# Performance work log

Hardware: AMD Instinct MI355X
Metric: run time of the kernel (lower is better)

Reference implementation:

```python
import jax, jax.numpy as jnp
import numpy as np

NEG = -1e30  # log-space 'zero' (avoid actual -inf for stable grads)
BLANK = 1


def _ctc_single(logp, target, il, tl):
    # logp: [T, V] log-probabilities; target: [S] int; il, tl: scalar lengths
    T, V = logp.shape
    S = target.shape[0]
    L = 2 * S + 1
    # extended label sequence: blank, t0, blank, t1, ..., blank
    ext = jnp.full((L,), BLANK, dtype=target.dtype).at[1::2].set(target)
    prev2 = jnp.concatenate([jnp.full((2,), -1, dtype=ext.dtype), ext[:-2]])
    can_skip = (ext != BLANK) & (ext != prev2)  # allowed s-2 transition
    valid = jnp.arange(L) < (2 * tl + 1)  # mask lattice positions beyond target length
    lp_ext = logp[:, ext]  # [T, L] gather of emission log-probs along the lattice

    alpha0 = jnp.full((L,), NEG, dtype=logp.dtype)
    alpha0 = alpha0.at[0].set(lp_ext[0, 0]).at[1].set(lp_ext[0, 1])
    alpha0 = jnp.where(valid, alpha0, NEG)

    def step(alpha, inp):
        t, lp = inp  # lp: [L]
        a1 = jnp.concatenate([jnp.full((1,), NEG, alpha.dtype), alpha[:-1]])
        a2 = jnp.concatenate([jnp.full((2,), NEG, alpha.dtype), alpha[:-2]])
        a2 = jnp.where(can_skip, a2, NEG)
        new = jnp.logaddexp(jnp.logaddexp(alpha, a1), a2) + lp
        new = jnp.where(valid, new, NEG)
        new = jnp.where(t < il, new, alpha)  # freeze alpha past input length
        return new, None

    alpha, _ = jax.lax.scan(step, alpha0, (jnp.arange(1, T), lp_ext[1:]))
    end = 2 * tl
    ll = jnp.logaddexp(alpha[end], alpha[end - 1])
    loss = -ll
    # zero_infinity=True: clamp non-finite / degenerate losses to 0
    loss = jnp.where(loss < 1e29, loss, 0.0)
    return loss


def setup_inputs() -> dict:
    key = jax.random.key(0)
    k1, k2, k3, k4 = jax.random.split(key, 4)
    B, T, V, S = 64, 2000, 256, 400
    # module expects log-probabilities over phonemes
    log_probs = jax.nn.log_softmax(
        jax.random.normal(k1, (B, T, V), dtype=jnp.float32), axis=-1)
    # targets avoid blank_id=1 (labels in [2, V))
    targets = jax.random.randint(k2, (B, S), 2, V, dtype=jnp.int32)
    input_lengths = jax.random.randint(k3, (B,), T // 2, T + 1, dtype=jnp.int32)
    target_lengths = jax.random.randint(k4, (B,), S // 2, S + 1, dtype=jnp.int32)
    return {"log_probs": log_probs, "targets": targets,
            "input_lengths": input_lengths, "target_lengths": target_lengths}


def reference(log_probs, targets, input_lengths, target_lengths):
    losses = jax.vmap(_ctc_single)(log_probs, targets, input_lengths, target_lengths)
    # nn.CTCLoss reduction='mean': per-sample loss divided by target length, then batch mean
    return jnp.mean(losses / target_lengths.astype(losses.dtype))
```

## Files before the change

kernel.cpp:

```cpp
#include <hip/hip_runtime.h>

#define LOG2E 1.4426950408889634f
#define LN2   0.6931471805599453f

namespace {
constexpr int B    = 64;
constexpr int T    = 2000;
constexpr int V    = 256;
constexpr int S    = 400;
constexpr int CHK  = 8;
constexpr int NCTP = 250;
constexpr int KP   = 408;
constexpr size_t GELEM  = (size_t)B * NCTP * KP * 8;
constexpr size_t GBYTES = GELEM * 2;
constexpr size_t LAOFF  = GBYTES / 4;
constexpr size_t LGOFF  = LAOFF + 64 * 1024;
constexpr size_t REQBYTES = GBYTES + 2 * 64 * 1024 * 4;
constexpr int LSTR = 260;
constexpr int NW7  = 7;
constexpr int NCT7 = 250;
constexpr int BST7 = 12;
}

using h8 = __attribute__((ext_vector_type(8))) _Float16;

__device__ __forceinline__ float fexp2(float x){ return __builtin_amdgcn_exp2f(x); }
__device__ __forceinline__ float flog2(float x){ return __builtin_amdgcn_logf(x); }

__device__ __forceinline__ float wave_shr1(float x) {
  int v = __builtin_amdgcn_update_dpp(0, __builtin_bit_cast(int, x),
                                      0x138, 0xf, 0xf, true);
  return __builtin_bit_cast(float, v);
}
__device__ __forceinline__ int wave_shr1_i(int x) {
  return __builtin_amdgcn_update_dpp(0, x, 0x138, 0xf, 0xf, true);
}
__device__ __forceinline__ float wave_shl1(float x) {
  int v = __builtin_amdgcn_update_dpp(0, __builtin_bit_cast(int, x),
                                      0x130, 0xf, 0xf, true);
  return __builtin_bit_cast(float, v);
}
__device__ __forceinline__ int wave_shl1_i(int x) {
  return __builtin_amdgcn_update_dpp(0, x, 0x130, 0xf, 0xf, true);
}

__global__ __launch_bounds__(512)
void ctc_gather_kernel(const float* __restrict__ logp,
                       const int* __restrict__ targets,
                       _Float16* __restrict__ G)
{
  const int tile = blockIdx.x;
  const int b    = blockIdx.y;
  const int tid  = threadIdx.x;
  const int i0   = tile * 64;
  const float* lp = logp + (size_t)b * T * V;
  const int*   tg = targets + (size_t)b * S;

  __shared__ float ls[64 * LSTR];
  __shared__ int   tgs[S];

  for (int f = tid; f < 64 * 64; f += 512) {
    const int row = f >> 6, c4 = f & 63;
    int t = i0 + 1 + row; if (t > T - 1) t = T - 1;
    float4 v = ((const float4*)(lp + (size_t)t * V))[c4];
    *(float4*)&ls[row * LSTR + c4 * 4] = v;
  }
  for (int k = tid; k < S; k += 512) tgs[k] = tg[k];
  __syncthreads();

  const int w    = tid >> 6;
  const int lane = tid & 63;
  _Float16* gb = G + (size_t)b * NCTP * KP * 8;

  for (int it = w; it < 56; it += 8) {
    const int kb = it >> 3;
    const int cc = it & 7;
    const int c  = tile * 8 + cc;
    if (c >= NCTP) continue;
    const int k = kb * 64 + lane;
    if (k >= KP) continue;
    const int e = (k < S) ? tgs[k] : 1;
    h8 hv;
    #pragma unroll
    for (int j = 0; j < 8; ++j)
      hv[j] = (_Float16)fexp2(ls[(cc * 8 + j) * LSTR + e] * LOG2E);
    *(h8*)(gb + ((size_t)c * KP + k) * 8) = hv;
  }
}

__global__ __launch_bounds__(64)
void ctc_fb_kernel(const float* __restrict__ logp,
                   const int* __restrict__ targets,
                   const int* __restrict__ input_len,
                   const int* __restrict__ target_len,
                   const _Float16* __restrict__ G,
                   float* __restrict__ la,
                   float* __restrict__ lg)
{
  const int b    = blockIdx.x;
  const int dir  = blockIdx.y;
  const int lane = threadIdx.x & 63;
  const float* __restrict__ lp = logp + (size_t)b * T * V;
  const int il = input_len[b];
  const int tl = target_len[b];
  const int m  = il >> 1;
  const int* tg = targets + (size_t)b * S;

  const _Float16* Gb = G + (size_t)b * NCTP * KP * 8;
  const int krow = (8 * lane < KP - 8) ? 8 * lane : KP - 8;

  float skF[8], skB[8];
  #pragma unroll
  for (int j = 0; j < 8; ++j) {
    const int k   = 8 * lane + j;
    const int kc  = k < S ? k : S - 1;
    const int km  = (k - 1) < 0 ? 0 : ((k - 1) < S ? (k - 1) : S - 1);
    skF[j] = (k > 0 && tg[kc] != tg[km]) ? 1.0f : 0.0f;
    const int k2  = k + 1;
    const int k2c = k2 < S ? k2 : S - 1;
    const int k2m = (k2 - 1) < S ? (k2 - 1) : S - 1;
    skB[j] = (tg[k2c] != tg[k2m]) ? 1.0f : 0.0f;
  }

  h8 bufA[9], bufB[9], bufC[9], bufD[9];

  auto loadch = [&](h8 (&buf)[9], int c2) {
    if (c2 < 0) c2 = 0;
    if (c2 > NCTP - 1) c2 = NCTP - 1;
    const size_t base = (size_t)c2 * (KP * 8);
    #pragma unroll
    for (int j = 0; j < 8; ++j)
      buf[j] = *(const h8*)(Gb + base + (size_t)(krow + j) * 8);
    buf[8] = *(const h8*)(Gb + base + (size_t)400 * 8);
  };

  if (dir == 0) {
    float a[16];
    #pragma unroll
    for (int i = 0; i < 16; ++i) a[i] = 0.0f;
    int  E = 0;
    bool alive = (lane == 0);
    if (lane == 0) {
      a[0] = fexp2(lp[1] * LOG2E);
      a[1] = fexp2(lp[tg[0]] * LOG2E);
    }

    auto fwd_sub = [&](h8 (&buf)[9], const int c_) {
      float ps[8][8], pb[8];
      #pragma unroll
      for (int j = 0; j < 8; ++j) {
        #pragma unroll
        for (int i = 0; i < 8; ++i) ps[j][i] = (float)buf[j][i];
      }
      #pragma unroll
      for (int i = 0; i < 8; ++i) pb[i] = (float)buf[8][i];
      loadch(buf, c_ + 4);

      const int E1 = wave_shr1_i(E);
      if (!alive) E = E1;
      int d = E1 - E; d = d > 126 ? 126 : (d < -126 ? -126 : d);
      const float f = ldexpf(1.0f, d);

      #pragma unroll
      for (int i = 0; i < 8; ++i) {
        const int t = 1 + c_ * CHK + i;
        if (t <= m) {
          const float h = wave_shr1(a[15]) * f;
          #pragma unroll
          for (int j = 7; j >= 0; --j) {
            const float lo = j ? a[2 * j - 1] : h;
            a[2 * j + 1] = __builtin_fmaf(lo, skF[j],
                                          a[2 * j + 1] + a[2 * j]) * ps[j][i];
            a[2 * j]     = (a[2 * j] + lo) * pb[i];
          }
        }
      }
      {
        float mx[8];
        #pragma unroll
        for (int q = 0; q < 8; ++q) mx[q] = fmaxf(a[2 * q], a[2 * q + 1]);
        #pragma unroll
        for (int q = 0; q < 4; ++q) mx[q] = fmaxf(mx[q], mx[q + 4]);
        const float m2 = fmaxf(fmaxf(mx[0], mx[1]), fmaxf(mx[2], mx[3]));
        int k = 0; (void)frexpf(m2, &k);
        #pragma unroll
        for (int i = 0; i < 16; ++i) a[i] = ldexpf(a[i], -k);
        E += k;
        alive = (m2 != 0.0f);
      }
    };

    loadch(bufA, 0); loadch(bufB, 1); loadch(bufC, 2); loadch(bufD, 3);
    const int NCH = (m + 7) >> 3;
    for (int c = 0; c < NCH; c += 4) {
      fwd_sub(bufA, c);
      fwd_sub(bufB, c + 1);
      fwd_sub(bufC, c + 2);
      fwd_sub(bufD, c + 3);
    }

    float* dst = la + (size_t)b * 1024 + 16 * lane;
    #pragma unroll
    for (int i = 0; i < 16; ++i) dst[i] = flog2(a[i]) + (float)E;
  } else {
    float g[16];
    const int s0 = 16 * lane;
    bool alive = false;
    #pragma unroll
    for (int i = 0; i < 16; ++i) {
      const int s = s0 + i;
      g[i] = (s == 2 * tl || s == 2 * tl - 1) ? 1.0f : 0.0f;
      alive = alive || (g[i] != 0.0f);
    }
    int E = 0;

    const int c_hi = (il - 2) >> 3;
    const int c_lo = m >> 3;

    auto bwd_sub = [&](h8 (&buf)[9], const int c_) {
      float ps[8][8], pb[8];
      #pragma unroll
      for (int j = 0; j < 8; ++j) {
        #pragma unroll
        for (int i = 0; i < 8; ++i) ps[j][i] = (float)buf[j][i];
      }
      #pragma unroll
      for (int i = 0; i < 8; ++i) pb[i] = (float)buf[8][i];
      loadch(buf, c_ - 4);

      const int E1 = wave_shl1_i(E);
      if (!alive) E = E1;
      int d = E1 - E; d = d > 126 ? 126 : (d < -126 ? -126 : d);
      const float f = ldexpf(1.0f, d);

      #pragma unroll
      for (int ii = 0; ii < 8; ++ii) {
        const int i = 7 - ii;
        const int row = 1 + c_ * CHK + i;
        if (row > m && row < il) {
          float pg[16];
          #pragma unroll
          for (int q = 0; q < 8; ++q) {
            pg[2 * q]     = g[2 * q]     * pb[i];
            pg[2 * q + 1] = g[2 * q + 1] * ps[q][i];
          }
          const float h0 = wave_shl1(pg[0]) * f;
          const float h1 = wave_shl1(pg[1]) * f;
          #pragma unroll
          for (int q = 0; q < 8; ++q) {
            const float u1 = (q < 7) ? pg[2 * q + 2] : h0;
            const float u2 = (q < 7) ? pg[2 * q + 3] : h1;
            g[2 * q + 1] = __builtin_fmaf(u2, skB[q], pg[2 * q + 1] + u1);
            g[2 * q]     = pg[2 * q] + pg[2 * q + 1];
          }
        }
      }
      {
        float mx[8];
        #pragma unroll
        for (int q = 0; q < 8; ++q) mx[q] = fmaxf(g[2 * q], g[2 * q + 1]);
        #pragma unroll
        for (int q = 0; q < 4; ++q) mx[q] = fmaxf(mx[q], mx[q + 4]);
        const float m2 = fmaxf(fmaxf(mx[0], mx[1]), fmaxf(mx[2], mx[3]));
        int k = 0; (void)frexpf(m2, &k);
        #pragma unroll
        for (int i = 0; i < 16; ++i) g[i] = ldexpf(g[i], -k);
        E += k;
        alive = (m2 != 0.0f);
      }
    };

    loadch(bufA, c_hi);     loadch(bufB, c_hi - 1);
    loadch(bufC, c_hi - 2); loadch(bufD, c_hi - 3);
    for (int c = c_hi; c >= c_lo; c -= 4) {
      bwd_sub(bufA, c);
      bwd_sub(bufB, c - 1);
      bwd_sub(bufC, c - 2);
      bwd_sub(bufD, c - 3);
    }

    float* dst = lg + (size_t)b * 1024 + 16 * lane;
    #pragma unroll
    for (int i = 0; i < 16; ++i) dst[i] = flog2(g[i]) + (float)E;
  }
}

__global__ __launch_bounds__(64)
void ctc_merge_kernel(const float* __restrict__ la,
                      const float* __restrict__ lg,
                      const int* __restrict__ target_len,
                      float* __restrict__ out)
{
  const int b    = blockIdx.x;
  const int lane = threadIdx.x;
  const int tl = target_len[b];
  const int Lb = 2 * tl + 1;
  const float* A  = la + (size_t)b * 1024;
  const float* Gm = lg + (size_t)b * 1024;

  float vs[16];
  float vmax = -1e30f;
  #pragma unroll
  for (int r = 0; r < 16; ++r) {
    const int s = lane + 64 * r;
    float x = A[s] + Gm[s];
    x = (s < Lb) ? x : -1e30f;
    vs[r] = x;
    vmax = fmaxf(vmax, x);
  }
  #pragma unroll
  for (int o = 32; o > 0; o >>= 1) vmax = fmaxf(vmax, __shfl_xor(vmax, o, 64));
  float sum = 0.0f;
  #pragma unroll
  for (int r = 0; r < 16; ++r) sum += fexp2(vs[r] - vmax);
  #pragma unroll
  for (int o = 32; o > 0; o >>= 1) sum += __shfl_xor(sum, o, 64);
  if (lane == 0) {
    const float ll = (vmax + flog2(sum)) * LN2;
    float loss = -ll;
    if (!(loss < 1e29f)) loss = 0.0f;
    atomicAdd(out, loss / ((float)tl * (float)B));
  }
}

__global__ __launch_bounds__(NW7 * 64)
void ctc_alpha7_kernel(const float* __restrict__ logp,
                       const int* __restrict__ targets,
                       const int* __restrict__ input_len,
                       const int* __restrict__ target_len,
                       float* __restrict__ out)
{
  const int b    = blockIdx.x;
  const int tid  = threadIdx.x;
  const int w    = tid >> 6;
  const int lane = tid & 63;
  const bool lane0 = (lane == 0);
  const float* __restrict__ lp = logp + (size_t)b * T * V;
  const int il = input_len[b];
  const int tl = target_len[b];
  const int Lb = 2 * tl + 1;

  __shared__ float bnd[NW7 - 1][NCT7 * BST7];
  __shared__ int   cnt[NW7 - 1];
  __shared__ float pblk[T];
  __shared__ float afin[NW7 * 64 * 2];

  if (tid < NW7 - 1) cnt[tid] = 0;

  const int* tg = targets + (size_t)b * S;
  const int k1 = (tid < S) ? tid : (S - 1);
  const int e1 = tg[k1];
  const float sk1 = (k1 == 0 || e1 != tg[k1 - 1]) ? 1.0f : 0.0f;

  for (int i = tid; i < T; i += NW7 * 64) {
    int t = (i + 1 < T) ? (i + 1) : (T - 1);
    pblk[i] = fexp2(lp[(size_t)t * V + 1] * LOG2E);
  }
  __syncthreads();

  const bool active = (w * 128) < Lb;
  if (active) {
    float a0 = 0.0f, a1 = 0.0f;
    int   E  = 0;
    if (tid == 0) { a0 = fexp2(lp[1] * LOG2E); a1 = fexp2(lp[e1] * LOG2E); }

    float tokL[CHK];
    #pragma unroll
    for (int i = 0; i < CHK; ++i) tokL[i] = lp[(size_t)(1 + i) * V + e1];

    const int NCH = (il - 1 + CHK - 1) / CHK;
    for (int c = 0; c < NCH; ++c) {
      const int t0 = 1 + c * CHK;
      float tokP[CHK];
      #pragma unroll
      for (int i = 0; i < CHK; ++i) tokP[i] = fexp2(tokL[i] * LOG2E);
      float nl[CHK];
      if (c + 1 < NCT7) {
        #pragma unroll
        for (int i = 0; i < CHK; ++i) {
          int tt = t0 + CHK + i; if (tt > T - 1) tt = T - 1;
          nl[i] = lp[(size_t)tt * V + e1];
        }
      }
      float pbk[CHK];
      {
        float4 q0 = *(const float4*)&pblk[c * CHK];
        float4 q1 = *(const float4*)&pblk[c * CHK + 4];
        pbk[0]=q0.x; pbk[1]=q0.y; pbk[2]=q0.z; pbk[3]=q0.w;
        pbk[4]=q1.x; pbk[5]=q1.y; pbk[6]=q1.z; pbk[7]=q1.w;
      }
      float bq[CHK];
      int Ep = 0;
      if (w > 0) {
        while (__hip_atomic_load(&cnt[w - 1], __ATOMIC_ACQUIRE,
                                 __HIP_MEMORY_SCOPE_WORKGROUP) < c + 1)
          __builtin_amdgcn_s_sleep(1);
        const float* src = &bnd[w - 1][c * BST7];
        float4 q0 = *(const float4*)(src);
        float4 q1 = *(const float4*)(src + 4);
        bq[0]=q0.x; bq[1]=q0.y; bq[2]=q0.z; bq[3]=q0.w;
        bq[4]=q1.x; bq[5]=q1.y; bq[6]=q1.z; bq[7]=q1.w;
        Ep = __float_as_int(src[8]);
      } else {
        #pragma unroll
        for (int i = 0; i < CHK; ++i) bq[i] = 0.0f;
      }
      const float mz  = fmaxf(a0, a1);
      const int   E1o = __shfl_up(E, 1);
      const int   E8  = __shfl_up(E, 8);
      const int   E9  = __shfl_up(E, 9);
      const float mz1 = __shfl_up(mz, 1);
      if (mz == 0.0f) E = (lane < 8) ? Ep : E8;
      int E1 = (mz1 == 0.0f) ? ((lane <= 8) ? Ep : E9) : E1o;
      if (lane0) E1 = (w == 0) ? E : Ep;
      int d = E1 - E; d = d > 126 ? 126 : (d < -126 ? -126 : d);
      const float f = ldexpf(1.0f, d);
      const float a1s = a1;
      float pub[CHK];
      #pragma unroll
      for (int i = 0; i < CHK; ++i) {
        const int t = t0 + i;
        if (t < il) {
          float hl = wave_shr1(a1);
          hl = lane0 ? bq[i] : hl;
          hl *= f;
          float s01 = a1 + a0;
          a1 = __builtin_fmaf(hl, sk1, s01) * tokP[i];
          a0 = (a0 + hl) * pbk[i];
        }
        pub[i] = a1;
      }
      if (w < NW7 - 1 && lane == 63) {
        float* dst = &bnd[w][c * BST7];
        dst[0] = a1s;
        #pragma unroll
        for (int i = 0; i < CHK - 1; ++i) dst[1 + i] = pub[i];
        dst[8] = __int_as_float(E);
        __hip_atomic_store(&cnt[w], c + 1, __ATOMIC_RELEASE,
                           __HIP_MEMORY_SCOPE_WORKGROUP);
      }
      {
        float m2 = fmaxf(a0, a1);
        int k = 0;
        (void)frexpf(m2, &k);
        a0 = ldexpf(a0, -k);
        a1 = ldexpf(a1, -k);
        E += k;
      }
      #pragma unroll
      for (int i = 0; i < CHK; ++i) tokL[i] = nl[i];
    }
    afin[2 * tid]     = flog2(a0) + (float)E;
    afin[2 * tid + 1] = flog2(a1) + (float)E;
  }
  __syncthreads();

  if (tid == 0) {
    const float x = afin[2 * tl];
    const float y = afin[2 * tl - 1];
    const float mm = fmaxf(x, y);
    const float ll = (mm + flog2(fexp2(x - mm) + fexp2(y - mm))) * LN2;
    float loss = -ll;
    if (!(loss < 1e29f)) loss = 0.0f;
    atomicAdd(out, loss / ((float)tl * (float)B));
  }
}

__global__ void ctc_zero_kernel(float* __restrict__ out) { out[0] = 0.0f; }

extern "C" void kernel_launch(void* const* d_in, const int* in_sizes, int n_in,
                              void* d_out, int out_size, void* d_ws, size_t ws_size,
                              hipStream_t stream) {
  const float* logp    = (const float*)d_in[0];
  const int*   targets = (const int*)d_in[1];
  const int*   il      = (const int*)d_in[2];
  const int*   tl      = (const int*)d_in[3];
  float* out = (float*)d_out;

  ctc_zero_kernel<<<1, 1, 0, stream>>>(out);
  if (ws_size >= REQBYTES) {
    _Float16* G  = (_Float16*)d_ws;
    float*    la = (float*)d_ws + LAOFF;
    float*    lg = (float*)d_ws + LGOFF;
    ctc_gather_kernel<<<dim3(32, B), 512, 0, stream>>>(logp, targets, G);
    ctc_fb_kernel<<<dim3(B, 2), 64, 0, stream>>>(logp, targets, il, tl, G, la, lg);
    ctc_merge_kernel<<<B, 64, 0, stream>>>(la, lg, tl, out);
  } else {
    ctc_alpha7_kernel<<<B, NW7 * 64, 0, stream>>>(logp, targets, il, tl, out);
  }
}
```

Before: 346.1 us.

## Stage emission chunks through an 8-deep LDS ring via global_load_lds

Replaces the four register-held prefetch buffers in the forward/backward recursion with an 8-slot shared-memory ring filled by direct global-to-LDS loads, using manual vmcnt/lgkmcnt waits and an XOR swizzle to avoid bank conflicts. The goal is to deepen prefetch to hide global latency and cut VGPR pressure from holding 36 h8 registers. It adds LDS reads per chunk and relies on hand-tuned waitcnt values, which are fragile if the compiler issues other memory ops.

```diff
diff --git a/kernel.cpp b/kernel.cpp
--- a/kernel.cpp
+++ b/kernel.cpp
@@ -20,6 +20,7 @@
 constexpr int NW7  = 7;
 constexpr int NCT7 = 250;
 constexpr int BST7 = 12;
+constexpr int SLOTR = 448;
 }
 
 using h8 = __attribute__((ext_vector_type(8))) _Float16;
@@ -43,6 +44,10 @@
 __device__ __forceinline__ int wave_shl1_i(int x) {
   return __builtin_amdgcn_update_dpp(0, x, 0x130, 0xf, 0xf, true);
 }
+
+#define WAITVM49() asm volatile("s_waitcnt vmcnt(49)" ::: "memory")
+#define WAITVM0()  asm volatile("s_waitcnt vmcnt(0)"  ::: "memory")
+#define WAITLGKM() asm volatile("s_waitcnt lgkmcnt(0)" ::: "memory")
 
 __global__ __launch_bounds__(512)
 void ctc_gather_kernel(const float* __restrict__ logp,
@@ -122,16 +127,32 @@
     skB[j] = (tg[k2c] != tg[k2m]) ? 1.0f : 0.0f;
   }
 
-  h8 bufA[9], bufB[9], bufC[9], bufD[9];
-
-  auto loadch = [&](h8 (&buf)[9], int c2) {
-    if (c2 < 0) c2 = 0;
-    if (c2 > NCTP - 1) c2 = NCTP - 1;
-    const size_t base = (size_t)c2 * (KP * 8);
-    #pragma unroll
-    for (int j = 0; j < 8; ++j)
-      buf[j] = *(const h8*)(Gb + base + (size_t)(krow + j) * 8);
-    buf[8] = *(const h8*)(Gb + base + (size_t)400 * 8);
+  __shared__ _Float16 ring[8][SLOTR * 8];
+
+  auto stage = [&](int chunk, int slot) {
+    if (chunk < 0) chunk = 0;
+    if (chunk > NCTP - 1) chunk = NCTP - 1;
+    const _Float16* src = Gb + (size_t)chunk * (KP * 8);
+    #pragma unroll
+    for (int q = 0; q < 7; ++q) {
+      const int p = q * 64 + lane;
+      int gr = p ^ ((p >> 3) & 7);
+      if (gr > KP - 1) gr = 400;
+      __builtin_amdgcn_global_load_lds(src + (size_t)gr * 8,
+                                       &ring[slot][(size_t)q * 64 * 8],
+                                       16, 0, 0);
+    }
+  };
+
+  auto rdchunk = [&](int slot, h8 (&cur)[9]) {
+    const _Float16* sl = &ring[slot][0];
+    #pragma unroll
+    for (int j = 0; j < 8; ++j) {
+      const int r = krow + j;
+      const int q = r ^ ((r >> 3) & 7);
+      cur[j] = *(const h8*)(sl + (size_t)q * 8);
+    }
+    cur[8] = *(const h8*)(sl + (size_t)402 * 8);
   };
 
   if (dir == 0) {
@@ -145,16 +166,19 @@
       a[1] = fexp2(lp[tg[0]] * LOG2E);
     }
 
-    auto fwd_sub = [&](h8 (&buf)[9], const int c_) {
-      float ps[8][8], pb[8];
-      #pragma unroll
-      for (int j = 0; j < 8; ++j) {
-        #pragma unroll
-        for (int i = 0; i < 8; ++i) ps[j][i] = (float)buf[j][i];
-      }
-      #pragma unroll
-      for (int i = 0; i < 8; ++i) pb[i] = (float)buf[8][i];
-      loadch(buf, c_ + 4);
+    h8 cur[9];
+    WAITVM0();
+    #pragma unroll
+    for (int k0 = 0; k0 < 8; ++k0) stage(k0, k0);
+    WAITVM49();
+    __builtin_amdgcn_sched_barrier(0);
+    rdchunk(0, cur);
+    WAITLGKM();
+    __builtin_amdgcn_sched_barrier(0);
+
+    const int NCH = (m + 7) >> 3;
+    for (int n = 0; n < NCH; ++n) {
+      stage(n + 8, n & 7);
 
       const int E1 = wave_shr1_i(E);
       if (!alive) E = E1;
@@ -163,15 +187,17 @@
 
       #pragma unroll
       for (int i = 0; i < 8; ++i) {
-        const int t = 1 + c_ * CHK + i;
+        const int t = 1 + n * CHK + i;
         if (t <= m) {
+          const float pbi = (float)cur[8][i];
           const float h = wave_shr1(a[15]) * f;
           #pragma unroll
           for (int j = 7; j >= 0; --j) {
+            const float psj = (float)cur[j][i];
             const float lo = j ? a[2 * j - 1] : h;
             a[2 * j + 1] = __builtin_fmaf(lo, skF[j],
-                                          a[2 * j + 1] + a[2 * j]) * ps[j][i];
-            a[2 * j]     = (a[2 * j] + lo) * pb[i];
+                                          a[2 * j + 1] + a[2 * j]) * psj;
+            a[2 * j]     = (a[2 * j] + lo) * pbi;
           }
         }
       }
@@ -188,15 +214,12 @@
         E += k;
         alive = (m2 != 0.0f);
       }
-    };
-
-    loadch(bufA, 0); loadch(bufB, 1); loadch(bufC, 2); loadch(bufD, 3);
-    const int NCH = (m + 7) >> 3;
-    for (int c = 0; c < NCH; c += 4) {
-      fwd_sub(bufA, c);
-      fwd_sub(bufB, c + 1);
-      fwd_sub(bufC, c + 2);
-      fwd_sub(bufD, c + 3);
+
+      WAITVM49();
+      __builtin_amdgcn_sched_barrier(0);
+      rdchunk((n + 1) & 7, cur);
+      WAITLGKM();
+      __builtin_amdgcn_sched_barrier(0);
     }
 
     float* dst = la + (size_t)b * 1024 + 16 * lane;
@@ -217,16 +240,18 @@
     const int c_hi = (il - 2) >> 3;
     const int c_lo = m >> 3;
 
-    auto bwd_sub = [&](h8 (&buf)[9], const int c_) {
-      float ps[8][8], pb[8];
-      #pragma unroll
-      for (int j = 0; j < 8; ++j) {
-        #pragma unroll
-        for (int i = 0; i < 8; ++i) ps[j][i] = (float)buf[j][i];
-      }
-      #pragma unroll
-      for (int i = 0; i < 8; ++i) pb[i] = (float)buf[8][i];
-      loadch(buf, c_ - 4);
+    h8 cur[9];
+    WAITVM0();
+    #pragma unroll
+    for (int k0 = 0; k0 < 8; ++k0) stage(c_hi - k0, (c_hi - k0) & 7);
+    WAITVM49();
+    __builtin_amdgcn_sched_barrier(0);
+    rdchunk(c_hi & 7, cur);
+    WAITLGKM();
+    __builtin_amdgcn_sched_barrier(0);
+
+    for (int n = c_hi; n >= c_lo; --n) {
+      stage(n - 8, (n - 8) & 7);
 
       const int E1 = wave_shl1_i(E);
       if (!alive) E = E1;
@@ -236,13 +261,14 @@
       #pragma unroll
       for (int ii = 0; ii < 8; ++ii) {
         const int i = 7 - ii;
-        const int row = 1 + c_ * CHK + i;
+        const int row = 1 + n * CHK + i;
         if (row > m && row < il) {
+          const float pbi = (float)cur[8][i];
           float pg[16];
           #pragma unroll
           for (int q = 0; q < 8; ++q) {
-            pg[2 * q]     = g[2 * q]     * pb[i];
-            pg[2 * q + 1] = g[2 * q + 1] * ps[q][i];
+            pg[2 * q]     = g[2 * q]     * pbi;
+            pg[2 * q + 1] = g[2 * q + 1] * (float)cur[q][i];
           }
           const float h0 = wave_shl1(pg[0]) * f;
           const float h1 = wave_shl1(pg[1]) * f;
@@ -268,15 +294,12 @@
         E += k;
         alive = (m2 != 0.0f);
       }
-    };
-
-    loadch(bufA, c_hi);     loadch(bufB, c_hi - 1);
-    loadch(bufC, c_hi - 2); loadch(bufD, c_hi - 3);
-    for (int c = c_hi; c >= c_lo; c -= 4) {
-      bwd_sub(bufA, c);
-      bwd_sub(bufB, c - 1);
-      bwd_sub(bufC, c - 2);
-      bwd_sub(bufD, c - 3);
+
+      WAITVM49();
+      __builtin_amdgcn_sched_barrier(0);
+      rdchunk((n - 1) & 7, cur);
+      WAITLGKM();
+      __builtin_amdgcn_sched_barrier(0);
     }
 
     float* dst = lg + (size_t)b * 1024 + 16 * lane;
```

Measured after the change: 371.1 us. 7.2% more time.

## Interleave emission table layout for coalesced loads and shrink prefetch depth

Applied to the files above, without the earlier changes.

Changes the per-chunk fp16 emission table layout so that entry j of each lane's eight labels is stored at j*51+lane, which makes each of the eight per-lane loads in the forward/backward kernels contiguous across lanes instead of strided by 8. The prefetch ring is cut from four chunk buffers to two, and the fp16-to-float conversion moves from an up-front unpacked array into the inner recurrence. These changes aim to reduce memory transactions and register pressure in the serial scan. The cost is a shorter prefetch distance, which may expose load latency.

```diff
diff --git a/kernel.cpp b/kernel.cpp
--- a/kernel.cpp
+++ b/kernel.cpp
@@ -72,19 +72,19 @@
   const int lane = tid & 63;
   _Float16* gb = G + (size_t)b * NCTP * KP * 8;
 
-  for (int it = w; it < 56; it += 8) {
-    const int kb = it >> 3;
-    const int cc = it & 7;
+  for (int it = w; it < 64; it += 8) {
+    const int cc = it >> 3;
+    const int j  = it & 7;
     const int c  = tile * 8 + cc;
     if (c >= NCTP) continue;
-    const int k = kb * 64 + lane;
-    if (k >= KP) continue;
+    if (lane > 50) continue;
+    const int k = 8 * lane + j;
     const int e = (k < S) ? tgs[k] : 1;
     h8 hv;
     #pragma unroll
-    for (int j = 0; j < 8; ++j)
-      hv[j] = (_Float16)fexp2(ls[(cc * 8 + j) * LSTR + e] * LOG2E);
-    *(h8*)(gb + ((size_t)c * KP + k) * 8) = hv;
+    for (int jj = 0; jj < 8; ++jj)
+      hv[jj] = (_Float16)fexp2(ls[(cc * 8 + jj) * LSTR + e] * LOG2E);
+    *(h8*)(gb + ((size_t)c * KP + j * 51 + lane) * 8) = hv;
   }
 }
 
@@ -107,7 +107,7 @@
   const int* tg = targets + (size_t)b * S;
 
   const _Float16* Gb = G + (size_t)b * NCTP * KP * 8;
-  const int krow = (8 * lane < KP - 8) ? 8 * lane : KP - 8;
+  const int lclamp = (lane < 50) ? lane : 50;
 
   float skF[8], skB[8];
   #pragma unroll
@@ -122,16 +122,16 @@
     skB[j] = (tg[k2c] != tg[k2m]) ? 1.0f : 0.0f;
   }
 
-  h8 bufA[9], bufB[9], bufC[9], bufD[9];
+  h8 bufA[9], bufB[9];
 
   auto loadch = [&](h8 (&buf)[9], int c2) {
     if (c2 < 0) c2 = 0;
     if (c2 > NCTP - 1) c2 = NCTP - 1;
-    const size_t base = (size_t)c2 * (KP * 8);
+    const _Float16* src = Gb + (size_t)c2 * (KP * 8);
     #pragma unroll
     for (int j = 0; j < 8; ++j)
-      buf[j] = *(const h8*)(Gb + base + (size_t)(krow + j) * 8);
-    buf[8] = *(const h8*)(Gb + base + (size_t)400 * 8);
+      buf[j] = *(const h8*)(src + (size_t)(j * 51 + lclamp) * 8);
+    buf[8] = *(const h8*)(src + (size_t)50 * 8);
   };
 
   if (dir == 0) {
@@ -146,15 +146,10 @@
     }
 
     auto fwd_sub = [&](h8 (&buf)[9], const int c_) {
-      float ps[8][8], pb[8];
-      #pragma unroll
-      for (int j = 0; j < 8; ++j) {
-        #pragma unroll
-        for (int i = 0; i < 8; ++i) ps[j][i] = (float)buf[j][i];
-      }
-      #pragma unroll
-      for (int i = 0; i < 8; ++i) pb[i] = (float)buf[8][i];
-      loadch(buf, c_ + 4);
+      h8 cur[9];
+      #pragma unroll
+      for (int r = 0; r < 9; ++r) cur[r] = buf[r];
+      loadch(buf, c_ + 2);
 
       const int E1 = wave_shr1_i(E);
       if (!alive) E = E1;
@@ -165,13 +160,15 @@
       for (int i = 0; i < 8; ++i) {
         const int t = 1 + c_ * CHK + i;
         if (t <= m) {
+          const float pbi = (float)cur[8][i];
           const float h = wave_shr1(a[15]) * f;
           #pragma unroll
           for (int j = 7; j >= 0; --j) {
+            const float psj = (float)cur[j][i];
             const float lo = j ? a[2 * j - 1] : h;
             a[2 * j + 1] = __builtin_fmaf(lo, skF[j],
-                                          a[2 * j + 1] + a[2 * j]) * ps[j][i];
-            a[2 * j]     = (a[2 * j] + lo) * pb[i];
+                                          a[2 * j + 1] + a[2 * j]) * psj;
+            a[2 * j]     = (a[2 * j] + lo) * pbi;
           }
         }
       }
@@ -190,13 +187,11 @@
       }
     };
 
-    loadch(bufA, 0); loadch(bufB, 1); loadch(bufC, 2); loadch(bufD, 3);
+    loadch(bufA, 0); loadch(bufB, 1);
     const int NCH = (m + 7) >> 3;
-    for (int c = 0; c < NCH; c += 4) {
+    for (int c = 0; c < NCH; c += 2) {
       fwd_sub(bufA, c);
       fwd_sub(bufB, c + 1);
-      fwd_sub(bufC, c + 2);
-      fwd_sub(bufD, c + 3);
     }
 
     float* dst = la + (size_t)b * 1024 + 16 * lane;
@@ -218,15 +213,10 @@
     const int c_lo = m >> 3;
 
     auto bwd_sub = [&](h8 (&buf)[9], const int c_) {
-      float ps[8][8], pb[8];
-      #pragma unroll
-      for (int j = 0; j < 8; ++j) {
-        #pragma unroll
-        for (int i = 0; i < 8; ++i) ps[j][i] = (float)buf[j][i];
-      }
-      #pragma unroll
-      for (int i = 0; i < 8; ++i) pb[i] = (float)buf[8][i];
-      loadch(buf, c_ - 4);
+      h8 cur[9];
+      #pragma unroll
+      for (int r = 0; r < 9; ++r) cur[r] = buf[r];
+      loadch(buf, c_ - 2);
 
       const int E1 = wave_shl1_i(E);
       if (!alive) E = E1;
@@ -238,11 +228,12 @@
         const int i = 7 - ii;
         const int row = 1 + c_ * CHK + i;
         if (row > m && row < il) {
+          const float pbi = (float)cur[8][i];
           float pg[16];
           #pragma unroll
           for (int q = 0; q < 8; ++q) {
-            pg[2 * q]     = g[2 * q]     * pb[i];
-            pg[2 * q + 1] = g[2 * q + 1] * ps[q][i];
+            pg[2 * q]     = g[2 * q]     * pbi;
+            pg[2 * q + 1] = g[2 * q + 1] * (float)cur[q][i];
           }
           const float h0 = wave_shl1(pg[0]) * f;
           const float h1 = wave_shl1(pg[1]) * f;
@@ -270,13 +261,10 @@
       }
     };
 
-    loadch(bufA, c_hi);     loadch(bufB, c_hi - 1);
-    loadch(bufC, c_hi - 2); loadch(bufD, c_hi - 3);
-    for (int c = c_hi; c >= c_lo; c -= 4) {
+    loadch(bufA, c_hi); loadch(bufB, c_hi - 1);
+    for (int c = c_hi; c >= c_lo; c -= 2) {
       bwd_sub(bufA, c);
       bwd_sub(bufB, c - 1);
-      bwd_sub(bufC, c - 2);
-      bwd_sub(bufD, c - 3);
     }
 
     float* dst = lg + (size_t)b * 1024 + 16 * lane;
```

Measured after the change: 341.4 us. No clear change (-1.4%).
